# Kernel optimization log

Hardware: AMD Instinct MI355X
Metric: run time of the kernel (lower is better)

The kernel has to match this reference:

```python
import jax, jax.numpy as jnp
import numpy as np

B, S, HID = 4, 1024, 2048
H, KV, D = 16, 4, 128  # query heads, kv heads, head_dim
ROPE_THETA = 1e6


def setup_inputs() -> dict:
    key = jax.random.key(0)
    ks = jax.random.split(key, 5)
    x = jax.random.normal(ks[0], (B, S, HID), dtype=jnp.float32)
    wq = jax.random.normal(ks[1], (HID, H * D), dtype=jnp.float32) / np.sqrt(HID)
    wk = jax.random.normal(ks[2], (HID, KV * D), dtype=jnp.float32) / np.sqrt(HID)
    wv = jax.random.normal(ks[3], (HID, KV * D), dtype=jnp.float32) / np.sqrt(HID)
    wo = jax.random.normal(ks[4], (H * D, HID), dtype=jnp.float32) / np.sqrt(H * D)
    # RoPE tables: freqs duplicated to head_dim (HF convention matching rotate_half)
    inv_freq = 1.0 / (ROPE_THETA ** (jnp.arange(0, D, 2, dtype=jnp.float32) / D))
    ang = jnp.arange(S, dtype=jnp.float32)[:, None] * inv_freq[None, :]  # [S, D/2]
    emb = jnp.concatenate([ang, ang], axis=-1)  # [S, D]
    return {"x": x, "cos": jnp.cos(emb), "sin": jnp.sin(emb),
            "wq": wq, "wk": wk, "wv": wv, "wo": wo}


def _rotate_half(t):
    half = t.shape[-1] // 2
    return jnp.concatenate([-t[..., half:], t[..., :half]], axis=-1)


def reference(x, cos, sin, wq, wk, wv, wo):
    b, s, _ = x.shape
    q = (x @ wq).reshape(b, s, H, D)
    k = (x @ wk).reshape(b, s, KV, D)
    v = (x @ wv).reshape(b, s, KV, D)
    # RoPE: cos/sin [S,D] broadcast over heads (unsqueeze_dim=1 -> [S,1,D])
    c = cos[:, None, :]
    sn = sin[:, None, :]
    q = q * c + _rotate_half(q) * sn
    k = k * c + _rotate_half(k) * sn
    # repeat_kv: each kv head repeated n_repeat times consecutively
    rep = H // KV
    k = jnp.repeat(k, rep, axis=2)  # [B,S,H,D]
    v = jnp.repeat(v, rep, axis=2)
    # [B,H,S,D]
    q = q.transpose(0, 2, 1, 3)
    k = k.transpose(0, 2, 1, 3)
    v = v.transpose(0, 2, 1, 3)
    scores = jnp.einsum("bhqd,bhkd->bhqk", q, k) / jnp.sqrt(jnp.float32(D))
    causal = jnp.tril(jnp.ones((s, s), dtype=bool))
    scores = jnp.where(causal, scores, -jnp.inf)
    probs = jax.nn.softmax(scores.astype(jnp.float32), axis=-1).astype(q.dtype)
    out = jnp.einsum("bhqk,bhkd->bhqd", probs, v)
    out = out.transpose(0, 2, 1, 3).reshape(b, s, H * D)
    return out @ wo
```

## Files before the change

### kernel.cpp

```cpp
#include <hip/hip_runtime.h>

typedef __attribute__((ext_vector_type(8))) __bf16 bf16x8;
typedef __attribute__((ext_vector_type(4))) __bf16 bf16x4;
typedef __attribute__((ext_vector_type(4))) float f32x4;

#define DEV static __device__ __forceinline__

DEV void gload_lds16(const void* g, void* l) {
  __builtin_amdgcn_global_load_lds((const __attribute__((address_space(1))) void*)g,
                                   (__attribute__((address_space(3))) void*)l, 16, 0, 0);
}

__global__ void cvt_kernel(const float* __restrict__ src, __bf16* __restrict__ dst, int n) {
  int i = (blockIdx.x * 256 + threadIdx.x) * 8;
  if (i >= n) return;
  float4 a = *(const float4*)(src + i);
  float4 b = *(const float4*)(src + i + 4);
  bf16x8 o;
  o[0] = (__bf16)a.x; o[1] = (__bf16)a.y; o[2] = (__bf16)a.z; o[3] = (__bf16)a.w;
  o[4] = (__bf16)b.x; o[5] = (__bf16)b.y; o[6] = (__bf16)b.z; o[7] = (__bf16)b.w;
  *(bf16x8*)(dst + i) = o;
}

__global__ void tcvt_kernel(const float* __restrict__ src, __bf16* __restrict__ dst, int K, int N) {
  __shared__ float tile[32][33];
  int k0 = blockIdx.y * 32, n0 = blockIdx.x * 32;
  int tx = threadIdx.x & 31, ty = threadIdx.x >> 5;
  #pragma unroll
  for (int i = 0; i < 32; i += 8)
    tile[ty + i][tx] = src[(size_t)(k0 + ty + i) * N + n0 + tx];
  __syncthreads();
  #pragma unroll
  for (int i = 0; i < 32; i += 8)
    dst[(size_t)(n0 + ty + i) * K + k0 + tx] = (__bf16)tile[tx][ty + i];
}

__global__ void vt_kernel(const __bf16* __restrict__ QKV, __bf16* __restrict__ VT) {
  __shared__ __bf16 t[32][33];
  int sx = blockIdx.x;
  int dx = blockIdx.y;
  int bk = blockIdx.z;
  int b = bk >> 2, kvh = bk & 3;
  int tx = threadIdx.x & 31, ty = threadIdx.x >> 5;
  #pragma unroll
  for (int i = 0; i < 32; i += 8)
    t[ty + i][tx] = QKV[(size_t)(b * 1024 + sx * 32 + ty + i) * 3072 + 2560 + kvh * 128 + dx * 32 + tx];
  __syncthreads();
  #pragma unroll
  for (int i = 0; i < 32; i += 8)
    VT[((size_t)bk * 128 + dx * 32 + ty + i) * 1024 + sx * 32 + tx] = t[tx][ty + i];
}

#define BM 128
#define BN 128
#define BKK 32

template <typename OutT>
__global__ __launch_bounds__(256, 4) void gemm_bt(const __bf16* __restrict__ A,
                                                  const __bf16* __restrict__ Bt,
                                                  OutT* __restrict__ C, int M, int N, int K) {
  __shared__ __bf16 As[2][BM * BKK];
  __shared__ __bf16 Bs[2][BM * BKK];
  const int tid = threadIdx.x;
  const int l = tid & 63;
  const int wid = tid >> 6;
  const int wr = wid >> 1, wc = wid & 1;

  const int nbx = gridDim.x;
  const int nwg = nbx * gridDim.y;
  int lin = blockIdx.y * nbx + blockIdx.x;
  if ((nwg & 7) == 0) lin = (lin & 7) * (nwg >> 3) + (lin >> 3);
  const int brow = (lin / nbx) * BM, bcol = (lin % nbx) * BN;

  const int g = l >> 4, ln = l & 15;

  f32x4 acc[4][4] = {};

  const int NT = K / BKK;

  auto stage = [&](int buf, int kt) {
    #pragma unroll
    for (int i = 0; i < 2; ++i) {
      int row = i * 64 + (tid >> 2);
      int kk = (tid & 3) * 8;
      int kksw = kk ^ (((row >> 1) & 3) * 8);
      gload_lds16(A + (size_t)(brow + row) * K + kt * BKK + kksw,
                  (char*)&As[buf][0] + i * 4096 + tid * 16);
      gload_lds16(Bt + (size_t)(bcol + row) * K + kt * BKK + kksw,
                  (char*)&Bs[buf][0] + i * 4096 + tid * 16);
    }
  };

  stage(0, 0);
  stage(1, 1);
  int cur = 0;
  for (int t = 0; t < NT; ++t) {
    if (t + 1 < NT) {
      asm volatile("s_waitcnt vmcnt(4)" ::: "memory");
    } else {
      asm volatile("s_waitcnt vmcnt(0)" ::: "memory");
    }
    __builtin_amdgcn_sched_barrier(0);
    __builtin_amdgcn_s_barrier();
    __builtin_amdgcn_sched_barrier(0);

    bf16x8 af[4], bfr[4];
    #pragma unroll
    for (int m = 0; m < 4; ++m) {
      int row = wr * 64 + m * 16 + ln;
      af[m] = *(const bf16x8*)((const char*)&As[cur][0] + row * 64 +
                               ((g * 8) ^ (((row >> 1) & 3) * 8)) * 2);
    }
    #pragma unroll
    for (int n = 0; n < 4; ++n) {
      int row = wc * 64 + n * 16 + ln;
      bfr[n] = *(const bf16x8*)((const char*)&Bs[cur][0] + row * 64 +
                                ((g * 8) ^ (((row >> 1) & 3) * 8)) * 2);
    }
    __builtin_amdgcn_s_setprio(1);
    #pragma unroll
    for (int m = 0; m < 4; ++m)
      #pragma unroll
      for (int n = 0; n < 4; ++n)
        acc[m][n] = __builtin_amdgcn_mfma_f32_16x16x32_bf16(af[m], bfr[n], acc[m][n], 0, 0, 0);
    __builtin_amdgcn_s_setprio(0);

    __builtin_amdgcn_sched_barrier(0);
    __builtin_amdgcn_s_barrier();
    __builtin_amdgcn_sched_barrier(0);
    if (t + 2 < NT) stage(cur, t + 2);
    cur ^= 1;
  }
  #pragma unroll
  for (int m = 0; m < 4; ++m)
    #pragma unroll
    for (int n = 0; n < 4; ++n)
      #pragma unroll
      for (int j = 0; j < 4; ++j) {
        size_t r = brow + wr * 64 + m * 16 + g * 4 + j;
        size_t c = bcol + wc * 64 + n * 16 + ln;
        C[r * N + c] = (OutT)acc[m][n][j];
      }
}

__global__ void rope_kernel(__bf16* __restrict__ QKV, const float* __restrict__ cosb,
                            const float* __restrict__ sinb) {
  int gid = blockIdx.x * 256 + threadIdx.x;
  int p = gid & 15;
  int ht = gid >> 4;
  int hc = ht % 20;
  int tok = ht / 20;
  int s = tok & 1023;
  int colb = hc < 16 ? hc * 128 : 2048 + (hc - 16) * 128;
  __bf16* base = QKV + (size_t)tok * 3072 + colb;
  int d0 = p * 4;
  const float* cr = cosb + s * 128;
  const float* sr = sinb + s * 128;
  float x0[4], x1[4];
  #pragma unroll
  for (int j = 0; j < 4; ++j) {
    x0[j] = (float)base[d0 + j];
    x1[j] = (float)base[d0 + 64 + j];
  }
  #pragma unroll
  for (int j = 0; j < 4; ++j) {
    float n0 = x0[j] * cr[d0 + j] - x1[j] * sr[d0 + j];
    float n1 = x1[j] * cr[d0 + 64 + j] + x0[j] * sr[d0 + 64 + j];
    base[d0 + j] = (__bf16)n0;
    base[d0 + 64 + j] = (__bf16)n1;
  }
}

__global__ __launch_bounds__(256, 2) void attn_kernel(const __bf16* __restrict__ QKV,
                                                      const __bf16* __restrict__ VT,
                                                      __bf16* __restrict__ AO) {
  __shared__ __bf16 Kl[2][64 * 128];
  __shared__ __bf16 Vt[128 * 64];
  __shared__ __bf16 Pl[4][16 * 72];

  const int tid = threadIdx.x, l = tid & 63, w = tid >> 6;
  const int h = blockIdx.y, b = blockIdx.z;
  const int kvh = h >> 2;
  const int g = l >> 4, ln = l & 15;
  const __bf16* VTg = VT + (size_t)(b * 4 + kvh) * 128 * 1024;
  const float scsc = 0.08838834764831845f;

  auto stageK = [&](int buf, int kt) {
    const __bf16* Kg = QKV + (size_t)(b * 1024 + kt * 64) * 3072 + 2048 + kvh * 128;
    #pragma unroll
    for (int i = 0; i < 4; ++i) {
      int r = i * 16 + (tid >> 4);
      int c = tid & 15;
      int csw = c ^ (r & 7);
      gload_lds16(Kg + (size_t)r * 3072 + csw * 8, (char*)&Kl[buf][0] + i * 4096 + tid * 16);
    }
  };
  auto stageV = [&](int kt) {
    #pragma unroll
    for (int i = 0; i < 4; ++i) {
      int ci = i * 256 + tid;
      int row = ci >> 3;
      int c = ci & 7;
      int csw = c ^ (row & 7);
      gload_lds16(VTg + (size_t)row * 1024 + kt * 64 + csw * 8, (char*)Vt + (size_t)ci * 16);
    }
  };

  #pragma unroll 1
  for (int pass = 0; pass < 2; ++pass) {
    const int qt = pass ? 15 - (int)blockIdx.x : (int)blockIdx.x;
    const size_t tokQ = (size_t)b * 1024 + qt * 64;

    bf16x8 qf[4];
    {
      const __bf16* qp = QKV + (tokQ + w * 16 + ln) * 3072 + h * 128;
      #pragma unroll
      for (int ks = 0; ks < 4; ++ks) qf[ks] = *(const bf16x8*)(qp + ks * 32 + g * 8);
    }

    float mrow = -1e30f, lrow = 0.f;
    f32x4 acco[8] = {};

    stageK(0, 0);
    int cur = 0;

    for (int kt = 0; kt <= qt; ++kt) {
      __syncthreads();

      stageV(kt);
      if (kt < qt) stageK(cur ^ 1, kt + 1);

      f32x4 accs[4] = {};
      __builtin_amdgcn_s_setprio(1);
      #pragma unroll
      for (int cb = 0; cb < 4; ++cb) {
        int row = cb * 16 + ln;
        #pragma unroll
        for (int ks = 0; ks < 4; ++ks) {
          bf16x8 kb = *(const bf16x8*)((const char*)&Kl[cur][0] + row * 256 +
                                       (((ks * 4 + g) ^ (row & 7)) * 16));
          accs[cb] = __builtin_amdgcn_mfma_f32_16x16x32_bf16(kb, qf[ks], accs[cb], 0, 0, 0);
        }
      }
      __builtin_amdgcn_s_setprio(0);

      const bool diag = (kt == qt);
      #pragma unroll
      for (int cb = 0; cb < 4; ++cb)
        #pragma unroll
        for (int j = 0; j < 4; ++j) {
          float s = accs[cb][j] * scsc;
          if (diag && (cb * 16 + g * 4 + j > w * 16 + ln)) s = -1e30f;
          accs[cb][j] = s;
        }

      float mt = accs[0][0];
      #pragma unroll
      for (int cb = 0; cb < 4; ++cb)
        #pragma unroll
        for (int j = 0; j < 4; ++j) mt = fmaxf(mt, accs[cb][j]);
      mt = fmaxf(mt, __shfl_xor(mt, 16, 64));
      mt = fmaxf(mt, __shfl_xor(mt, 32, 64));
      float mnew = fmaxf(mrow, mt);
      float corr = __expf(mrow - mnew);
      mrow = mnew;
      float rs = 0.f;
      #pragma unroll
      for (int cb = 0; cb < 4; ++cb)
        #pragma unroll
        for (int j = 0; j < 4; ++j) {
          float p = __expf(accs[cb][j] - mnew);
          accs[cb][j] = p;
          rs += p;
        }
      rs += __shfl_xor(rs, 16, 64);
      rs += __shfl_xor(rs, 32, 64);
      lrow = lrow * corr + rs;
      #pragma unroll
      for (int n = 0; n < 8; ++n)
        #pragma unroll
        for (int j = 0; j < 4; ++j) acco[n][j] *= corr;

      #pragma unroll
      for (int cb = 0; cb < 4; ++cb) {
        bf16x4 pw;
        #pragma unroll
        for (int j = 0; j < 4; ++j) pw[j] = (__bf16)accs[cb][j];
        *(bf16x4*)(&Pl[w][ln * 72 + cb * 16 + g * 4]) = pw;
      }

      __syncthreads();

      __builtin_amdgcn_s_setprio(1);
      #pragma unroll
      for (int sc = 0; sc < 2; ++sc) {
        bf16x8 pa = *(const bf16x8*)(&Pl[w][ln * 72 + sc * 32 + g * 8]);
        #pragma unroll
        for (int n = 0; n < 8; ++n) {
          int row = n * 16 + ln;
          bf16x8 vb = *(const bf16x8*)((const char*)Vt + row * 128 +
                                       (((sc * 4 + g) ^ (row & 7)) * 16));
          acco[n] = __builtin_amdgcn_mfma_f32_16x16x32_bf16(vb, pa, acco[n], 0, 0, 0);
        }
      }
      __builtin_amdgcn_s_setprio(0);
      cur ^= 1;
    }

    float rl = 1.f / lrow;
    size_t r = tokQ + w * 16 + ln;
    #pragma unroll
    for (int n = 0; n < 8; ++n) {
      bf16x4 ov;
      #pragma unroll
      for (int j = 0; j < 4; ++j) ov[j] = (__bf16)(acco[n][j] * rl);
      *(bf16x4*)(&AO[r * 2048 + h * 128 + n * 16 + g * 4]) = ov;
    }
  }
}

extern "C" void kernel_launch(void* const* d_in, const int* in_sizes, int n_in,
                              void* d_out, int out_size, void* d_ws, size_t ws_size,
                              hipStream_t stream) {
  const float* x    = (const float*)d_in[0];
  const float* cosb = (const float*)d_in[1];
  const float* sinb = (const float*)d_in[2];
  const float* wq   = (const float*)d_in[3];
  const float* wk   = (const float*)d_in[4];
  const float* wv   = (const float*)d_in[5];
  const float* wo   = (const float*)d_in[6];
  float* out = (float*)d_out;

  char* ws = (char*)d_ws;
  const size_t OFF_XB    = 0;
  const size_t OFF_WQKVT = OFF_XB + 16777216;
  const size_t OFF_WOT   = OFF_WQKVT + 12582912;
  const size_t OFF_QKV   = OFF_WOT + 8388608;
  const size_t OFF_AO    = OFF_QKV + 25165824;
  const size_t OFF_VT    = OFF_XB;

  __bf16* Xb    = (__bf16*)(ws + OFF_XB);
  __bf16* WqkvT = (__bf16*)(ws + OFF_WQKVT);
  __bf16* WoT   = (__bf16*)(ws + OFF_WOT);
  __bf16* QKVb  = (__bf16*)(ws + OFF_QKV);
  __bf16* AOb   = (__bf16*)(ws + OFF_AO);
  __bf16* VTb   = (__bf16*)(ws + OFF_VT);

  cvt_kernel<<<4096 * 2048 / 8 / 256, 256, 0, stream>>>(x, Xb, 4096 * 2048);
  tcvt_kernel<<<dim3(64, 64), 256, 0, stream>>>(wq, WqkvT, 2048, 2048);
  tcvt_kernel<<<dim3(16, 64), 256, 0, stream>>>(wk, WqkvT + (size_t)2048 * 2048, 2048, 512);
  tcvt_kernel<<<dim3(16, 64), 256, 0, stream>>>(wv, WqkvT + (size_t)2560 * 2048, 2048, 512);
  tcvt_kernel<<<dim3(64, 64), 256, 0, stream>>>(wo, WoT, 2048, 2048);
  gemm_bt<__bf16><<<dim3(3072 / BN, 4096 / BM), 256, 0, stream>>>(Xb, WqkvT, QKVb, 4096, 3072, 2048);
  vt_kernel<<<dim3(32, 4, 16), 256, 0, stream>>>(QKVb, VTb);
  rope_kernel<<<4096 * 20 * 16 / 256, 256, 0, stream>>>(QKVb, cosb, sinb);
  attn_kernel<<<dim3(8, 16, 4), 256, 0, stream>>>(QKVb, VTb, AOb);
  gemm_bt<float><<<dim3(2048 / BN, 4096 / BM), 256, 0, stream>>>(AOb, WoT, out, 4096, 2048, 2048);
}
```

Measured before the change: 192.7 us.

## Replace GEMMs with 8-wave 256-wide tiles and four-phase load/MFMA interleaving

Swaps the 128x128, 4-wave double-buffered GEMM for an 8-wave kernel with 256-column tiles (256 or 128 rows) and a K-step of 64. Each K-step is split into four compute phases, and the next stage's global-to-LDS loads are spread across those phases with fine-grained vmcnt waits. This is meant to raise MFMA utilisation by overlapping loads with math and to cut global traffic per FLOP through larger tiles. The cost is more LDS and registers per block, fewer blocks in flight, and a hardcoded `(kt+2)&31` wrap that assumes K=2048.

After: 175.3 us. -9.1%, faster.

```diff
diff --git a/kernel.cpp b/kernel.cpp
--- a/kernel.cpp
+++ b/kernel.cpp
@@ -9,6 +9,11 @@
 DEV void gload_lds16(const void* g, void* l) {
   __builtin_amdgcn_global_load_lds((const __attribute__((address_space(1))) void*)g,
                                    (__attribute__((address_space(3))) void*)l, 16, 0, 0);
+}
+
+DEV void lgkm0_sb() {
+  asm volatile("s_waitcnt lgkmcnt(0)" ::: "memory");
+  __builtin_amdgcn_sched_barrier(0);
 }
 
 __global__ void cvt_kernel(const float* __restrict__ src, __bf16* __restrict__ dst, int n) {
@@ -51,95 +56,182 @@
     VT[((size_t)bk * 128 + dx * 32 + ty + i) * 1024 + sx * 32 + tx] = t[tx][ty + i];
 }
 
-#define BM 128
-#define BN 128
-#define BKK 32
-
-template <typename OutT>
-__global__ __launch_bounds__(256, 4) void gemm_bt(const __bf16* __restrict__ A,
-                                                  const __bf16* __restrict__ Bt,
-                                                  OutT* __restrict__ C, int M, int N, int K) {
-  __shared__ __bf16 As[2][BM * BKK];
-  __shared__ __bf16 Bs[2][BM * BKK];
+template <int BM, typename OutT>
+__global__ __launch_bounds__(512, 2) void gemm8p(const __bf16* __restrict__ A,
+                                                 const __bf16* __restrict__ Bt,
+                                                 OutT* __restrict__ C,
+                                                 int M, int N, int K) {
+  constexpr int ABYTES = BM * 64 * 2;
+  constexpr int BBYTES = 256 * 64 * 2;
+  constexpr int MH = BM / 64;
+  __shared__ alignas(1024) char smem[2 * (ABYTES + BBYTES)];
+
   const int tid = threadIdx.x;
-  const int l = tid & 63;
-  const int wid = tid >> 6;
-  const int wr = wid >> 1, wc = wid & 1;
+  const int l = tid & 63, w = tid >> 6;
+  const int wr = w >> 2, wc = w & 3;
+  const int g = l >> 4, ln = l & 15;
 
   const int nbx = gridDim.x;
   const int nwg = nbx * gridDim.y;
   int lin = blockIdx.y * nbx + blockIdx.x;
-  if ((nwg & 7) == 0) lin = (lin & 7) * (nwg >> 3) + (lin >> 3);
-  const int brow = (lin / nbx) * BM, bcol = (lin % nbx) * BN;
-
-  const int g = l >> 4, ln = l & 15;
-
-  f32x4 acc[4][4] = {};
-
-  const int NT = K / BKK;
-
-  auto stage = [&](int buf, int kt) {
-    #pragma unroll
-    for (int i = 0; i < 2; ++i) {
-      int row = i * 64 + (tid >> 2);
-      int kk = (tid & 3) * 8;
-      int kksw = kk ^ (((row >> 1) & 3) * 8);
-      gload_lds16(A + (size_t)(brow + row) * K + kt * BKK + kksw,
-                  (char*)&As[buf][0] + i * 4096 + tid * 16);
-      gload_lds16(Bt + (size_t)(bcol + row) * K + kt * BKK + kksw,
-                  (char*)&Bs[buf][0] + i * 4096 + tid * 16);
-    }
-  };
-
-  stage(0, 0);
-  stage(1, 1);
-  int cur = 0;
-  for (int t = 0; t < NT; ++t) {
-    if (t + 1 < NT) {
-      asm volatile("s_waitcnt vmcnt(4)" ::: "memory");
+  lin = (lin & 7) * (nwg >> 3) + (lin >> 3);
+  const int brow = (lin / nbx) * BM, bcol = (lin % nbx) * 256;
+
+  const __bf16* Ag = A + (size_t)brow * K;
+  const __bf16* Bg = Bt + (size_t)bcol * K;
+  const int NT = K / 64;
+
+  auto Abuf = [&](int buf) -> char* { return smem + buf * ABYTES; };
+  auto Bbuf = [&](int buf) -> char* { return smem + 2 * ABYTES + buf * BBYTES; };
+
+  f32x4 acc[2 * MH][4] = {};
+
+  auto chunk = [&](const __bf16* gb, char* lb, int ktc, int sub) {
+    int r16 = l >> 2;
+    int colb = ((l & 3) * 16) ^ (((l >> 5) & 1) << 5);
+    int row = (sub >> 1) * 16 + r16;
+    gload_lds16(gb + (size_t)row * K + ktc * 64 + (sub & 1) * 32 + (colb >> 1),
+                lb + sub * 1024 + l * 16);
+  };
+  auto stA0 = [&](int ktc, int buf) {
+    if constexpr (BM == 256) {
+      #pragma unroll
+      for (int i = 0; i < 2; ++i) { int idx = i * 8 + w; chunk(Ag, Abuf(buf), ktc, (idx >> 3) * 16 + (idx & 7)); }
     } else {
-      asm volatile("s_waitcnt vmcnt(0)" ::: "memory");
-    }
+      chunk(Ag, Abuf(buf), ktc, (w >> 2) * 8 + (w & 3));
+    }
+  };
+  auto stA1 = [&](int ktc, int buf) {
+    if constexpr (BM == 256) {
+      #pragma unroll
+      for (int i = 0; i < 2; ++i) { int idx = i * 8 + w; chunk(Ag, Abuf(buf), ktc, 8 + (idx >> 3) * 16 + (idx & 7)); }
+    } else {
+      chunk(Ag, Abuf(buf), ktc, 4 + (w >> 2) * 8 + (w & 3));
+    }
+  };
+  auto stB0 = [&](int ktc, int buf) {
+    #pragma unroll
+    for (int i = 0; i < 2; ++i) { int idx = i * 8 + w; chunk(Bg, Bbuf(buf), ktc, (idx >> 2) * 8 + (idx & 3)); }
+  };
+  auto stB1 = [&](int ktc, int buf) {
+    #pragma unroll
+    for (int i = 0; i < 2; ++i) { int idx = i * 8 + w; chunk(Bg, Bbuf(buf), ktc, 4 + (idx >> 2) * 8 + (idx & 3)); }
+  };
+
+  auto ldA = [&](int buf, int m, int kk) -> bf16x8 {
+    int sub = (wr * (BM / 32) + m) * 2 + kk;
+    return *(const bf16x8*)(Abuf(buf) + sub * 1024 + ln * 64 + ((g * 16) ^ (((ln >> 3) & 1) << 5)));
+  };
+  auto ldB = [&](int buf, int n, int kk) -> bf16x8 {
+    int sub = (wc * 4 + n) * 2 + kk;
+    return *(const bf16x8*)(Bbuf(buf) + sub * 1024 + ln * 64 + ((g * 16) ^ (((ln >> 3) & 1) << 5)));
+  };
+
+  auto vmw = [&](int which) {
+    if constexpr (BM == 256) {
+      if (which == 0) asm volatile("s_waitcnt vmcnt(10)" ::: "memory");
+      else if (which == 1) asm volatile("s_waitcnt vmcnt(12)" ::: "memory");
+      else asm volatile("s_waitcnt vmcnt(12)" ::: "memory");
+    } else {
+      if (which == 0) asm volatile("s_waitcnt vmcnt(7)" ::: "memory");
+      else if (which == 1) asm volatile("s_waitcnt vmcnt(9)" ::: "memory");
+      else asm volatile("s_waitcnt vmcnt(9)" ::: "memory");
+    }
+    __builtin_amdgcn_sched_barrier(0);
+  };
+  auto bar = [&]() {
     __builtin_amdgcn_sched_barrier(0);
     __builtin_amdgcn_s_barrier();
     __builtin_amdgcn_sched_barrier(0);
-
-    bf16x8 af[4], bfr[4];
-    #pragma unroll
-    for (int m = 0; m < 4; ++m) {
-      int row = wr * 64 + m * 16 + ln;
-      af[m] = *(const bf16x8*)((const char*)&As[cur][0] + row * 64 +
-                               ((g * 8) ^ (((row >> 1) & 3) * 8)) * 2);
-    }
-    #pragma unroll
-    for (int n = 0; n < 4; ++n) {
-      int row = wc * 64 + n * 16 + ln;
-      bfr[n] = *(const bf16x8*)((const char*)&Bs[cur][0] + row * 64 +
-                                ((g * 8) ^ (((row >> 1) & 3) * 8)) * 2);
-    }
+  };
+
+  stA0(0, 0); stB0(0, 0); stB1(0, 0); stA1(0, 0);
+  stA0(1, 1); stB0(1, 1); stB1(1, 1); stA1(1, 1);
+  vmw(2);
+  bar();
+
+  bf16x8 af[MH][2], bf[4][2];
+
+  for (int kt = 0; kt < NT; ++kt) {
+    const int buf = kt & 1;
+    const int ktc = (kt + 2) & 31;
+
+    #pragma unroll
+    for (int m = 0; m < MH; ++m) { af[m][0] = ldA(buf, m, 0); af[m][1] = ldA(buf, m, 1); }
+    #pragma unroll
+    for (int n = 0; n < 2; ++n) { bf[n][0] = ldB(buf, n, 0); bf[n][1] = ldB(buf, n, 1); }
+    bar();
+    lgkm0_sb();
     __builtin_amdgcn_s_setprio(1);
     #pragma unroll
-    for (int m = 0; m < 4; ++m)
-      #pragma unroll
-      for (int n = 0; n < 4; ++n)
-        acc[m][n] = __builtin_amdgcn_mfma_f32_16x16x32_bf16(af[m], bfr[n], acc[m][n], 0, 0, 0);
+    for (int m = 0; m < MH; ++m)
+      #pragma unroll
+      for (int n = 0; n < 2; ++n)
+        #pragma unroll
+        for (int kk = 0; kk < 2; ++kk)
+          acc[m][n] = __builtin_amdgcn_mfma_f32_16x16x32_bf16(af[m][kk], bf[n][kk], acc[m][n], 0, 0, 0);
     __builtin_amdgcn_s_setprio(0);
-
-    __builtin_amdgcn_sched_barrier(0);
-    __builtin_amdgcn_s_barrier();
-    __builtin_amdgcn_sched_barrier(0);
-    if (t + 2 < NT) stage(cur, t + 2);
-    cur ^= 1;
+    vmw(0);
+    bar();
+
+    #pragma unroll
+    for (int n = 2; n < 4; ++n) { bf[n][0] = ldB(buf, n, 0); bf[n][1] = ldB(buf, n, 1); }
+    stA0(ktc, buf); stB0(ktc, buf);
+    bar();
+    lgkm0_sb();
+    __builtin_amdgcn_s_setprio(1);
+    #pragma unroll
+    for (int m = 0; m < MH; ++m)
+      #pragma unroll
+      for (int n = 2; n < 4; ++n)
+        #pragma unroll
+        for (int kk = 0; kk < 2; ++kk)
+          acc[m][n] = __builtin_amdgcn_mfma_f32_16x16x32_bf16(af[m][kk], bf[n][kk], acc[m][n], 0, 0, 0);
+    __builtin_amdgcn_s_setprio(0);
+    vmw(1);
+    bar();
+
+    #pragma unroll
+    for (int m = 0; m < MH; ++m) { af[m][0] = ldA(buf, MH + m, 0); af[m][1] = ldA(buf, MH + m, 1); }
+    stB1(ktc, buf);
+    bar();
+    lgkm0_sb();
+    __builtin_amdgcn_s_setprio(1);
+    #pragma unroll
+    for (int m = 0; m < MH; ++m)
+      #pragma unroll
+      for (int n = 0; n < 2; ++n)
+        #pragma unroll
+        for (int kk = 0; kk < 2; ++kk)
+          acc[MH + m][n] = __builtin_amdgcn_mfma_f32_16x16x32_bf16(af[m][kk], bf[n][kk], acc[MH + m][n], 0, 0, 0);
+    __builtin_amdgcn_s_setprio(0);
+    bar();
+
+    stA1(ktc, buf);
+    bar();
+    lgkm0_sb();
+    __builtin_amdgcn_s_setprio(1);
+    #pragma unroll
+    for (int m = 0; m < MH; ++m)
+      #pragma unroll
+      for (int n = 2; n < 4; ++n)
+        #pragma unroll
+        for (int kk = 0; kk < 2; ++kk)
+          acc[MH + m][n] = __builtin_amdgcn_mfma_f32_16x16x32_bf16(af[m][kk], bf[n][kk], acc[MH + m][n], 0, 0, 0);
+    __builtin_amdgcn_s_setprio(0);
+    vmw(2);
+    bar();
   }
-  #pragma unroll
-  for (int m = 0; m < 4; ++m)
+
+  #pragma unroll
+  for (int mi = 0; mi < 2 * MH; ++mi)
     #pragma unroll
     for (int n = 0; n < 4; ++n)
       #pragma unroll
       for (int j = 0; j < 4; ++j) {
-        size_t r = brow + wr * 64 + m * 16 + g * 4 + j;
+        size_t r = brow + wr * (BM / 2) + mi * 16 + g * 4 + j;
         size_t c = bcol + wc * 64 + n * 16 + ln;
-        C[r * N + c] = (OutT)acc[m][n][j];
+        C[r * N + c] = (OutT)acc[mi][n][j];
       }
 }
 
@@ -351,9 +443,9 @@
   tcvt_kernel<<<dim3(16, 64), 256, 0, stream>>>(wk, WqkvT + (size_t)2048 * 2048, 2048, 512);
   tcvt_kernel<<<dim3(16, 64), 256, 0, stream>>>(wv, WqkvT + (size_t)2560 * 2048, 2048, 512);
   tcvt_kernel<<<dim3(64, 64), 256, 0, stream>>>(wo, WoT, 2048, 2048);
-  gemm_bt<__bf16><<<dim3(3072 / BN, 4096 / BM), 256, 0, stream>>>(Xb, WqkvT, QKVb, 4096, 3072, 2048);
+  gemm8p<256, __bf16><<<dim3(12, 16), 512, 0, stream>>>(Xb, WqkvT, QKVb, 4096, 3072, 2048);
   vt_kernel<<<dim3(32, 4, 16), 256, 0, stream>>>(QKVb, VTb);
   rope_kernel<<<4096 * 20 * 16 / 256, 256, 0, stream>>>(QKVb, cosb, sinb);
   attn_kernel<<<dim3(8, 16, 4), 256, 0, stream>>>(QKVb, VTb, AOb);
-  gemm_bt<float><<<dim3(2048 / BN, 4096 / BM), 256, 0, stream>>>(AOb, WoT, out, 4096, 2048, 2048);
-}
+  gemm8p<128, float><<<dim3(8, 32), 512, 0, stream>>>(AOb, WoT, out, 4096, 2048, 2048);
+}
```
